# Optimization experiments

Hardware: AMD Instinct MI355X
Metric: run time of the kernel (lower is better)

The kernel has to match this reference:

```python
import jax, jax.numpy as jnp
import numpy as np

N_META, M_SUB = 64, 1024          # n meta-nodes, m nodes per sub-graph
D_IN, D_HID, D_OUT = 128, 128, 64
NUM_LAYERS_EXTRA, K = 2, 3        # total DSGraphGLayers = NUM_LAYERS_EXTRA + 1
N_EDGES = 1048576                 # ~avg degree 16 over 65536 nodes


def setup_inputs() -> dict:
    key = jax.random.key(0)
    ks = jax.random.split(key, 8)
    N = N_META * M_SUB
    x = jax.random.normal(ks[0], (N_META, M_SUB, D_IN), jnp.float32)
    sub_adj = jax.random.randint(ks[1], (2, N_EDGES), 0, N, dtype=jnp.int32)
    # dense binary meta-graph adjacency (n, n)
    adj = (jax.random.uniform(ks[2], (N_META, N_META)) < 0.1).astype(jnp.float32)
    L = NUM_LAYERS_EXTRA + 1
    scale = 1.0 / np.sqrt(D_HID).astype(np.float32)
    gcn_W = jax.random.normal(ks[3], (L, K + 1, D_HID, D_HID), jnp.float32) * scale
    gcn_b = jnp.zeros((L, K + 1, D_HID), jnp.float32)
    lin_W1 = jax.random.normal(ks[4], (D_HID, D_HID), jnp.float32) * scale
    lin_b1 = jnp.zeros((D_HID,), jnp.float32)
    lin_W2 = jax.random.normal(ks[5], (D_HID, D_OUT), jnp.float32) * scale
    lin_b2 = jnp.zeros((D_OUT,), jnp.float32)
    return dict(x=x, sub_adj=sub_adj, adj=adj, gcn_W=gcn_W, gcn_b=gcn_b,
                lin_W1=lin_W1, lin_b1=lin_b1, lin_W2=lin_W2, lin_b2=lin_b2)


def _gcn_conv(x, src, dst, dinv, W, b, N):
    norm = dinv[src] * dinv[dst]                      # [E+N]
    msg = (x @ W)[src] * norm[:, None]                # [E+N, d_out]
    return jax.ops.segment_sum(msg, dst, num_segments=N) + b


def reference(x, sub_adj, adj, gcn_W, gcn_b, lin_W1, lin_b1, lin_W2, lin_b2):
    n, m, d = x.shape
    N = n * m
    loops = jnp.arange(N, dtype=sub_adj.dtype)
    src = jnp.concatenate([sub_adj[0], loops])
    dst = jnp.concatenate([sub_adj[1], loops])
    deg = jax.ops.segment_sum(jnp.ones(src.shape, x.dtype), dst, num_segments=N)
    dinv = jnp.where(deg > 0, jax.lax.rsqrt(deg), jnp.zeros_like(deg))
    # precompute_adj: cached_adj = [adj, adj^2, ..., adj^K]; powers >= 2 detached in source
    cached = [adj]
    A = adj
    for _ in range(K - 1):
        A = jax.lax.stop_gradient(A @ adj)
        cached.append(A)
    for li in range(gcn_W.shape[0]):
        xf = x.reshape(N, -1)
        out = _gcn_conv(xf, src, dst, dinv, gcn_W[li, 0], gcn_b[li, 0], N)
        for i, Ai in enumerate(cached):
            # meta-graph mixing: x_i[n,m,d] = sum_j A_i[n,j] * x[j,m,d]
            xi = jnp.einsum('nj,jmd->nmd', Ai, x).reshape(N, -1)
            out = out + _gcn_conv(xi, src, dst, dinv, gcn_W[li, i + 1], gcn_b[li, i + 1], N)
        x = jax.nn.relu(out.reshape(n, m, -1))
    h = x.reshape(N, -1)
    h = jax.nn.relu(h @ lin_W1 + lin_b1)
    h = h @ lin_W2 + lin_b2
    return h.reshape(n, m, -1)
```

## Files before the change

kernel.cpp:

```cpp
#include <hip/hip_runtime.h>

#define NMETA 64
#define MSUB 1024
#define NNODES 65536
#define D 128
#define DOUT 64
#define NEDGES 1048576
#define COLS 131072
#define BCAP 5120

typedef __attribute__((ext_vector_type(8))) short bf8_t;
typedef __attribute__((ext_vector_type(4))) float f4_t;
typedef __attribute__((ext_vector_type(2))) float f2_t;

__device__ inline unsigned short bfr(float x) {
    unsigned u = __builtin_bit_cast(unsigned, x);
    u += 0x7fffu + ((u >> 16) & 1u);
    return (unsigned short)(u >> 16);
}
__device__ inline float b2f(unsigned short h) {
    return __builtin_bit_cast(float, (unsigned)h << 16);
}
__device__ inline f2_t up2(unsigned u) {
    f2_t r;
    r[0] = __builtin_bit_cast(float, u << 16);
    r[1] = __builtin_bit_cast(float, u & 0xffff0000u);
    return r;
}

__global__ __launch_bounds__(256) void k_bhist(const int* __restrict__ dst,
                                               int* __restrict__ whist) {
    __shared__ int c[256];
    int t = threadIdx.x, w = blockIdx.x;
    c[t] = 0;
    __syncthreads();
    const int* dp = dst + w * 4096;
    for (int k = 0; k < 16; ++k) atomicAdd(&c[dp[k * 256 + t] >> 8], 1);
    __syncthreads();
    whist[t * 256 + w] = c[t];
}

__global__ __launch_bounds__(256) void k_bscan(int* __restrict__ whist,
                                               int* __restrict__ bbase) {
    __shared__ int sh[256];
    int t = threadIdx.x;
    int run = 0;
    for (int w = 0; w < 256; ++w) {
        int v = whist[t * 256 + w];
        whist[t * 256 + w] = run;
        run += v;
    }
    sh[t] = run;
    __syncthreads();
    for (int d = 1; d < 256; d <<= 1) {
        int x = (t >= d) ? sh[t - d] : 0;
        __syncthreads();
        sh[t] += x;
        __syncthreads();
    }
    bbase[t] = sh[t] - run;
    if (t == 255) bbase[256] = NEDGES;
}

__global__ __launch_bounds__(256) void k_bscatter(const int* __restrict__ src,
                                                  const int* __restrict__ dst,
                                                  const int* __restrict__ bbase,
                                                  const int* __restrict__ whist,
                                                  unsigned* __restrict__ tmp) {
    __shared__ int cur[256];
    __shared__ int base[256];
    int t = threadIdx.x, w = blockIdx.x;
    cur[t] = 0;
    base[t] = bbase[t] + whist[t * 256 + w];
    __syncthreads();
    const int* dp = dst + w * 4096;
    const int* sp = src + w * 4096;
    for (int k = 0; k < 16; ++k) {
        int d = dp[k * 256 + t], s = sp[k * 256 + t];
        int b = d >> 8;
        int lr = atomicAdd(&cur[b], 1);
        tmp[base[b] + lr] = ((unsigned)(d & 255) << 16) | (unsigned)s;
    }
}

__global__ __launch_bounds__(256) void k_bcsr(const unsigned* __restrict__ tmp,
                                              const int* __restrict__ bbase,
                                              int* __restrict__ offs,
                                              float* __restrict__ dinv,
                                              unsigned short* __restrict__ csr16) {
    __shared__ unsigned pairs[BCAP];
    __shared__ unsigned short image[BCAP];
    __shared__ int cnt[256], cur[256], sh[256];
    int t = threadIdx.x, b = blockIdx.x;
    int base = bbase[b], n = bbase[b + 1] - base;
    for (int i = t; i < n; i += 256) pairs[i] = tmp[base + i];
    cnt[t] = 0;
    __syncthreads();
    for (int i = t; i < n; i += 256) atomicAdd(&cnt[pairs[i] >> 16], 1);
    __syncthreads();
    int c = cnt[t];
    sh[t] = c;
    __syncthreads();
    for (int d = 1; d < 256; d <<= 1) {
        int x = (t >= d) ? sh[t - d] : 0;
        __syncthreads();
        sh[t] += x;
        __syncthreads();
    }
    int excl = sh[t] - c;
    cur[t] = excl;
    offs[b * 256 + t] = base + excl;
    dinv[b * 256 + t] = rsqrtf((float)(c + 1));
    if (b == 255 && t == 255) offs[65536] = NEDGES;
    __syncthreads();
    for (int i = t; i < n; i += 256) {
        unsigned p = pairs[i];
        int pos = atomicAdd(&cur[p >> 16], 1);
        image[pos] = (unsigned short)(p & 0xffffu);
    }
    __syncthreads();
    for (int i = t; i < n; i += 256) csr16[base + i] = image[i];
}

__global__ __launch_bounds__(256) void k_setup(const float* __restrict__ A,
                                               unsigned short* __restrict__ Ab,
                                               const float4* __restrict__ x,
                                               ushort4* __restrict__ xo,
                                               const float* __restrict__ gcnW,
                                               const float* __restrict__ W1,
                                               const float* __restrict__ W2,
                                               unsigned short* __restrict__ Wt) {
    int blk = blockIdx.x, t = threadIdx.x;
    if (blk == 0) {
        __shared__ float As[4096];
        __shared__ float Bs[4096];
        for (int q = 0; q < 16; ++q) As[t + 256 * q] = A[t + 256 * q];
        __syncthreads();
        for (int q = 0; q < 16; ++q) {
            int idx = t + 256 * q;
            int n = idx >> 6, j = idx & 63;
            Ab[idx] = bfr(As[idx]);
            float acc = 0.f;
            for (int k = 0; k < 64; ++k) acc += As[n * 64 + k] * As[k * 64 + j];
            Bs[idx] = acc;
            Ab[4096 + idx] = bfr(acc);
        }
        __syncthreads();
        for (int q = 0; q < 16; ++q) {
            int idx = t + 256 * q;
            int n = idx >> 6, j = idx & 63;
            float acc = 0.f;
            for (int k = 0; k < 64; ++k) acc += Bs[n * 64 + k] * As[k * 64 + j];
            Ab[8192 + idx] = bfr(acc);
        }
    } else if (blk <= 8192) {
        int i = (blk - 1) * 256 + t;
        float4 v = x[i];
        ushort4 u;
        u.x = bfr(v.x); u.y = bfr(v.y); u.z = bfr(v.z); u.w = bfr(v.w);
        xo[i] = u;
    } else {
        int b2 = blk - 8193;
        int m = b2 >> 6;
        int idx = (b2 & 63) * 256 + t;
        const float* src;
        int N = 128;
        if (m < 12)       src = gcnW + m * 16384;
        else if (m == 12) src = W1;
        else { src = W2; N = 64; if (idx >= 8192) return; }
        int n = idx >> 7, k = idx & 127;
        Wt[m * 16384 + idx] = bfr(src[k * N + n]);
    }
}

#define TS 130
__global__ __launch_bounds__(256) void k_layer(const unsigned short* __restrict__ X,
                                               const unsigned short* __restrict__ Ab,
                                               const unsigned short* __restrict__ Wt4,
                                               unsigned short* __restrict__ Y) {
    __shared__ unsigned short LB[3 * 64 * TS];
    int t = threadIdx.x;
    int m = blockIdx.x;
    int wave = t >> 6, lane = t & 63;
    int l16 = lane & 15, kg = lane >> 4;
    int c0 = wave * 32;

#pragma unroll
    for (int it = 0; it < 4; ++it) {
        int slot = it * 256 + t;
        int row = slot >> 4, ch = slot & 15;
        *(uint4*)&LB[row * 128 + ch * 8] =
            *(const uint4*)(X + ((long)row * MSUB + m) * D + ch * 8);
    }
    __syncthreads();

    bf8_t xa[4][4];
#pragma unroll
    for (int mt = 0; mt < 4; ++mt)
#pragma unroll
        for (int kb = 0; kb < 4; ++kb)
            xa[mt][kb] = *(const bf8_t*)&LB[(mt * 16 + l16) * 128 + kb * 32 + kg * 8];
    __syncthreads();

    f4_t zero4 = {0.f, 0.f, 0.f, 0.f};

    f4_t accT0[4][2];
#pragma unroll
    for (int mt = 0; mt < 4; ++mt)
#pragma unroll
        for (int nt = 0; nt < 2; ++nt) accT0[mt][nt] = zero4;
#pragma unroll
    for (int kb = 0; kb < 4; ++kb)
#pragma unroll
        for (int nt = 0; nt < 2; ++nt) {
            bf8_t b = *(const bf8_t*)(Wt4 + (long)(c0 + nt * 16 + l16) * 128 +
                                      kb * 32 + kg * 8);
#pragma unroll
            for (int mt = 0; mt < 4; ++mt)
                accT0[mt][nt] = __builtin_amdgcn_mfma_f32_16x16x32_bf16(
                    xa[mt][kb], b, accT0[mt][nt], 0, 0, 0);
        }

#pragma unroll
    for (int z = 1; z < 4; ++z) {
        f4_t acc[4][2];
#pragma unroll
        for (int mt = 0; mt < 4; ++mt)
#pragma unroll
            for (int nt = 0; nt < 2; ++nt) acc[mt][nt] = zero4;
        const unsigned short* wp = Wt4 + z * 16384;
#pragma unroll
        for (int kb = 0; kb < 4; ++kb)
#pragma unroll
            for (int nt = 0; nt < 2; ++nt) {
                bf8_t b = *(const bf8_t*)(wp + (long)(c0 + nt * 16 + l16) * 128 +
                                          kb * 32 + kg * 8);
#pragma unroll
                for (int mt = 0; mt < 4; ++mt)
                    acc[mt][nt] = __builtin_amdgcn_mfma_f32_16x16x32_bf16(
                        xa[mt][kb], b, acc[mt][nt], 0, 0, 0);
            }
#pragma unroll
        for (int mt = 0; mt < 4; ++mt)
#pragma unroll
            for (int nt = 0; nt < 2; ++nt)
#pragma unroll
                for (int r = 0; r < 4; ++r)
                    LB[((z - 1) * 64 + mt * 16 + kg * 4 + r) * TS +
                       c0 + nt * 16 + l16] = bfr(acc[mt][nt][r]);
    }

    f4_t acc2[4][2];
#pragma unroll
    for (int mt = 0; mt < 4; ++mt)
#pragma unroll
        for (int nt = 0; nt < 2; ++nt) acc2[mt][nt] = zero4;
#pragma unroll
    for (int i = 0; i < 3; ++i)
#pragma unroll
        for (int kb = 0; kb < 2; ++kb) {
            bf8_t af[4];
#pragma unroll
            for (int mt = 0; mt < 4; ++mt)
                af[mt] = *(const bf8_t*)(Ab + i * 4096 + (mt * 16 + l16) * 64 +
                                         kb * 32 + kg * 8);
#pragma unroll
            for (int nt = 0; nt < 2; ++nt) {
                bf8_t b;
#pragma unroll
                for (int jj = 0; jj < 8; ++jj)
                    b[jj] = (short)LB[(i * 64 + kb * 32 + kg * 8 + jj) * TS +
                                      c0 + nt * 16 + l16];
#pragma unroll
                for (int mt = 0; mt < 4; ++mt)
                    acc2[mt][nt] = __builtin_amdgcn_mfma_f32_16x16x32_bf16(
                        af[mt], b, acc2[mt][nt], 0, 0, 0);
            }
        }

#pragma unroll
    for (int mt = 0; mt < 4; ++mt)
#pragma unroll
        for (int nt = 0; nt < 2; ++nt)
#pragma unroll
            for (int r = 0; r < 4; ++r) {
                int row = mt * 16 + kg * 4 + r;
                int col = c0 + nt * 16 + l16;
                float v = acc2[mt][nt][r] + accT0[mt][nt][r];
                Y[((long)row * MSUB + m) * D + col] = bfr(v);
            }
}

template <int NT, bool RELU, bool OUT_BF16>
__global__ __launch_bounds__(256) void k_mfma(const unsigned short* __restrict__ X,
                                              const unsigned short* __restrict__ Wt,
                                              const float* __restrict__ bias,
                                              void* __restrict__ Cout) {
    int wave = threadIdx.x >> 6, lane = threadIdx.x & 63;
    int l16 = lane & 15, kg = lane >> 4;
    long row0 = (long)blockIdx.x * 128 + wave * 32;
    const int NCOL = NT * 16;

    bf8_t a[2][4];
    const unsigned short* xp = X + row0 * 128 + kg * 8;
#pragma unroll
    for (int kb = 0; kb < 4; ++kb) {
        a[0][kb] = *(const bf8_t*)(xp + (long)l16 * 128 + kb * 32);
        a[1][kb] = *(const bf8_t*)(xp + (long)(l16 + 16) * 128 + kb * 32);
    }
    f4_t acc[2][NT];
    f4_t zero4 = {0.f, 0.f, 0.f, 0.f};
#pragma unroll
    for (int mt = 0; mt < 2; ++mt)
#pragma unroll
        for (int nt = 0; nt < NT; ++nt) acc[mt][nt] = zero4;

    const unsigned short* wp = Wt + (long)l16 * 128 + kg * 8;
#pragma unroll
    for (int kb = 0; kb < 4; ++kb)
#pragma unroll
        for (int nt = 0; nt < NT; ++nt) {
            bf8_t b = *(const bf8_t*)(wp + nt * 16 * 128 + kb * 32);
            acc[0][nt] = __builtin_amdgcn_mfma_f32_16x16x32_bf16(a[0][kb], b, acc[0][nt], 0, 0, 0);
            acc[1][nt] = __builtin_amdgcn_mfma_f32_16x16x32_bf16(a[1][kb], b, acc[1][nt], 0, 0, 0);
        }
#pragma unroll
    for (int mt = 0; mt < 2; ++mt)
#pragma unroll
        for (int nt = 0; nt < NT; ++nt)
#pragma unroll
            for (int r = 0; r < 4; ++r) {
                long row = row0 + mt * 16 + kg * 4 + r;
                int col = nt * 16 + l16;
                float v = acc[mt][nt][r] + bias[col];
                if (RELU) v = fmaxf(v, 0.f);
                long o = row * NCOL + col;
                if (OUT_BF16) ((unsigned short*)Cout)[o] = bfr(v);
                else          ((float*)Cout)[o] = v;
            }
}

__global__ __launch_bounds__(256) void k_prop(const unsigned short* __restrict__ Y,
                                              const int* __restrict__ offs,
                                              const unsigned short* __restrict__ csr,
                                              const float* __restrict__ dinv,
                                              const float* __restrict__ bias4,
                                              unsigned short* __restrict__ Xout) {
    int wid = threadIdx.x >> 6;
    int lane = threadIdx.x & 63;
    int q = lane >> 4;
    int l = lane & 15;
    int v = blockIdx.x * 4 + wid;
    const uint4* Y4 = (const uint4*)Y;
    int e0 = offs[v], e1 = offs[v + 1];
    f2_t acc2[4];
#pragma unroll
    for (int k = 0; k < 4; ++k) acc2[k] = (f2_t){0.f, 0.f};

    int e = e0 + q;
    for (; e + 4 < e1; e += 8) {
        int u0 = csr[e], u1 = csr[e + 4];
        float d0 = dinv[u0], d1 = dinv[u1];
        uint4 y0 = Y4[(long)u0 * 16 + l];
        uint4 y1 = Y4[(long)u1 * 16 + l];
        f2_t dd0 = {d0, d0}, dd1 = {d1, d1};
        acc2[0] += dd0 * up2(y0.x) + dd1 * up2(y1.x);
        acc2[1] += dd0 * up2(y0.y) + dd1 * up2(y1.y);
        acc2[2] += dd0 * up2(y0.z) + dd1 * up2(y1.z);
        acc2[3] += dd0 * up2(y0.w) + dd1 * up2(y1.w);
    }
    if (e < e1) {
        int u = csr[e];
        float du = dinv[u];
        uint4 y = Y4[(long)u * 16 + l];
        f2_t dd = {du, du};
        acc2[0] += dd * up2(y.x);
        acc2[1] += dd * up2(y.y);
        acc2[2] += dd * up2(y.z);
        acc2[3] += dd * up2(y.w);
    }
    float acc[8];
#pragma unroll
    for (int k = 0; k < 4; ++k) { acc[2 * k] = acc2[k][0]; acc[2 * k + 1] = acc2[k][1]; }
#pragma unroll
    for (int k = 0; k < 8; ++k) {
        acc[k] += __shfl_xor(acc[k], 32, 64);
        acc[k] += __shfl_xor(acc[k], 16, 64);
    }
    if (q == 0) {
        float dv = dinv[v];
        float dvv = dv * dv;
        uint4 s = Y4[(long)v * 16 + l];
        f2_t s2[4] = {up2(s.x), up2(s.y), up2(s.z), up2(s.w)};
        float bs[8];
#pragma unroll
        for (int k = 0; k < 8; ++k) bs[k] = 0.f;
#pragma unroll
        for (int p = 0; p < 4; ++p) {
            float4 blo = *(const float4*)(bias4 + p * 128 + l * 8);
            float4 bhi = *(const float4*)(bias4 + p * 128 + l * 8 + 4);
            bs[0] += blo.x; bs[1] += blo.y; bs[2] += blo.z; bs[3] += blo.w;
            bs[4] += bhi.x; bs[5] += bhi.y; bs[6] += bhi.z; bs[7] += bhi.w;
        }
        unsigned r[8];
#pragma unroll
        for (int k = 0; k < 8; ++k) {
            float sf = s2[k / 2][k % 2];
            r[k] = bfr(fmaxf(dv * acc[k] + dvv * sf + bs[k], 0.f));
        }
        uint4 pk;
        pk.x = (r[1] << 16) | r[0];
        pk.y = (r[3] << 16) | r[2];
        pk.z = (r[5] << 16) | r[4];
        pk.w = (r[7] << 16) | r[6];
        ((uint4*)Xout)[(long)v * 16 + l] = pk;
    }
}

extern "C" void kernel_launch(void* const* d_in, const int* in_sizes, int n_in,
                              void* d_out, int out_size, void* d_ws, size_t ws_size,
                              hipStream_t stream) {
    const float* x      = (const float*)d_in[0];
    const int*   subadj = (const int*)d_in[1];
    const float* adj    = (const float*)d_in[2];
    const float* gcn_W  = (const float*)d_in[3];
    const float* gcn_b  = (const float*)d_in[4];
    const float* lin_W1 = (const float*)d_in[5];
    const float* lin_b1 = (const float*)d_in[6];
    const float* lin_W2 = (const float*)d_in[7];
    const float* lin_b2 = (const float*)d_in[8];
    float* out = (float*)d_out;

    const int* e_src = subadj;
    const int* e_dst = subadj + NEDGES;

    char* w = (char*)d_ws;
    int*      whist = (int*)w;      w += (size_t)65536 * 4;
    int*      bbase = (int*)w;      w += (size_t)260 * 4;
    int*      offs  = (int*)w;      w += (size_t)65540 * 4;
    float*    dinv  = (float*)w;    w += (size_t)65536 * 4;
    unsigned* tmp   = (unsigned*)w; w += (size_t)NEDGES * 4;
    unsigned short* csr16 = (unsigned short*)w; w += (size_t)NEDGES * 2;
    unsigned short* Ab  = (unsigned short*)w; w += (size_t)3 * 4096 * 2;
    unsigned short* Xbf = (unsigned short*)w; w += (size_t)NNODES * D * 2;
    unsigned short* Ybf = (unsigned short*)w; w += (size_t)NNODES * D * 2;
    unsigned short* Wt  = (unsigned short*)w; w += (size_t)14 * 16384 * 2;
    unsigned short* Hbf = (unsigned short*)w; w += (size_t)NNODES * D * 2;

    k_bhist<<<256, 256, 0, stream>>>(e_dst, whist);
    k_bscan<<<1, 256, 0, stream>>>(whist, bbase);
    k_bscatter<<<256, 256, 0, stream>>>(e_src, e_dst, bbase, whist, tmp);
    k_bcsr<<<256, 256, 0, stream>>>(tmp, bbase, offs, dinv, csr16);
    k_setup<<<9089, 256, 0, stream>>>(adj, Ab, (const float4*)x, (ushort4*)Xbf,
                                      gcn_W, lin_W1, lin_W2, Wt);

    for (int li = 0; li < 3; ++li) {
        k_layer<<<MSUB, 256, 0, stream>>>(Xbf, Ab, Wt + (size_t)li * 4 * 16384, Ybf);
        k_prop<<<NNODES / 4, 256, 0, stream>>>(Ybf, offs, csr16, dinv,
                                               gcn_b + (size_t)li * 512, Xbf);
    }
    k_mfma<8, true, true><<<NNODES / 128, 256, 0, stream>>>(
        Xbf, Wt + (size_t)12 * 16384, lin_b1, Hbf);
    k_mfma<4, false, false><<<NNODES / 128, 256, 0, stream>>>(
        Hbf, Wt + (size_t)13 * 16384, lin_b2, out);
}
```

Measured before the change: 457.8 us.

## Fuse fp32-to-bf16 input conversion, prescale by dinv, and fuse MLP layers

Three changes. The fp32-to-bf16 conversion of x moves out of the setup kernel into the first layer's load. The source-side D^-1/2 normalization moves into the layer kernel's epilogue, so the edge-gather loop no longer loads dinv per neighbor, and that loop is unrolled to four neighbors. The two MLP GEMMs are fused into one kernel that keeps the hidden activations in shared memory. This removes a separate conversion pass, a random-access dinv load per edge, and a global round trip for H. The cost is an extra rounding of the prescaled Y to bf16 and more registers in the prop loop.

New measurement: 454.8 us. About the same (-0.7%).

```diff
diff --git a/kernel.cpp b/kernel.cpp
--- a/kernel.cpp
+++ b/kernel.cpp
@@ -124,8 +124,6 @@
 
 __global__ __launch_bounds__(256) void k_setup(const float* __restrict__ A,
                                                unsigned short* __restrict__ Ab,
-                                               const float4* __restrict__ x,
-                                               ushort4* __restrict__ xo,
                                                const float* __restrict__ gcnW,
                                                const float* __restrict__ W1,
                                                const float* __restrict__ W2,
@@ -153,14 +151,8 @@
             for (int k = 0; k < 64; ++k) acc += Bs[n * 64 + k] * As[k * 64 + j];
             Ab[8192 + idx] = bfr(acc);
         }
-    } else if (blk <= 8192) {
-        int i = (blk - 1) * 256 + t;
-        float4 v = x[i];
-        ushort4 u;
-        u.x = bfr(v.x); u.y = bfr(v.y); u.z = bfr(v.z); u.w = bfr(v.w);
-        xo[i] = u;
     } else {
-        int b2 = blk - 8193;
+        int b2 = blk - 1;
         int m = b2 >> 6;
         int idx = (b2 & 63) * 256 + t;
         const float* src;
@@ -174,23 +166,41 @@
 }
 
 #define TS 130
+template <bool INF32>
 __global__ __launch_bounds__(256) void k_layer(const unsigned short* __restrict__ X,
+                                               const float* __restrict__ Xf,
                                                const unsigned short* __restrict__ Ab,
                                                const unsigned short* __restrict__ Wt4,
+                                               const float* __restrict__ dinv,
                                                unsigned short* __restrict__ Y) {
     __shared__ unsigned short LB[3 * 64 * TS];
+    __shared__ float dsh[64];
     int t = threadIdx.x;
     int m = blockIdx.x;
     int wave = t >> 6, lane = t & 63;
     int l16 = lane & 15, kg = lane >> 4;
     int c0 = wave * 32;
 
+    if (t < 64) dsh[t] = dinv[(long)t * MSUB + m];
+
 #pragma unroll
     for (int it = 0; it < 4; ++it) {
         int slot = it * 256 + t;
         int row = slot >> 4, ch = slot & 15;
-        *(uint4*)&LB[row * 128 + ch * 8] =
-            *(const uint4*)(X + ((long)row * MSUB + m) * D + ch * 8);
+        if (INF32) {
+            const float* xp = Xf + ((long)row * MSUB + m) * D + ch * 8;
+            float4 va = *(const float4*)xp;
+            float4 vb = *(const float4*)(xp + 4);
+            uint4 pk;
+            pk.x = ((unsigned)bfr(va.y) << 16) | bfr(va.x);
+            pk.y = ((unsigned)bfr(va.w) << 16) | bfr(va.z);
+            pk.z = ((unsigned)bfr(vb.y) << 16) | bfr(vb.x);
+            pk.w = ((unsigned)bfr(vb.w) << 16) | bfr(vb.z);
+            *(uint4*)&LB[row * 128 + ch * 8] = pk;
+        } else {
+            *(uint4*)&LB[row * 128 + ch * 8] =
+                *(const uint4*)(X + ((long)row * MSUB + m) * D + ch * 8);
+        }
     }
     __syncthreads();
 
@@ -286,57 +296,8 @@
             for (int r = 0; r < 4; ++r) {
                 int row = mt * 16 + kg * 4 + r;
                 int col = c0 + nt * 16 + l16;
-                float v = acc2[mt][nt][r] + accT0[mt][nt][r];
+                float v = (acc2[mt][nt][r] + accT0[mt][nt][r]) * dsh[row];
                 Y[((long)row * MSUB + m) * D + col] = bfr(v);
-            }
-}
-
-template <int NT, bool RELU, bool OUT_BF16>
-__global__ __launch_bounds__(256) void k_mfma(const unsigned short* __restrict__ X,
-                                              const unsigned short* __restrict__ Wt,
-                                              const float* __restrict__ bias,
-                                              void* __restrict__ Cout) {
-    int wave = threadIdx.x >> 6, lane = threadIdx.x & 63;
-    int l16 = lane & 15, kg = lane >> 4;
-    long row0 = (long)blockIdx.x * 128 + wave * 32;
-    const int NCOL = NT * 16;
-
-    bf8_t a[2][4];
-    const unsigned short* xp = X + row0 * 128 + kg * 8;
-#pragma unroll
-    for (int kb = 0; kb < 4; ++kb) {
-        a[0][kb] = *(const bf8_t*)(xp + (long)l16 * 128 + kb * 32);
-        a[1][kb] = *(const bf8_t*)(xp + (long)(l16 + 16) * 128 + kb * 32);
-    }
-    f4_t acc[2][NT];
-    f4_t zero4 = {0.f, 0.f, 0.f, 0.f};
-#pragma unroll
-    for (int mt = 0; mt < 2; ++mt)
-#pragma unroll
-        for (int nt = 0; nt < NT; ++nt) acc[mt][nt] = zero4;
-
-    const unsigned short* wp = Wt + (long)l16 * 128 + kg * 8;
-#pragma unroll
-    for (int kb = 0; kb < 4; ++kb)
-#pragma unroll
-        for (int nt = 0; nt < NT; ++nt) {
-            bf8_t b = *(const bf8_t*)(wp + nt * 16 * 128 + kb * 32);
-            acc[0][nt] = __builtin_amdgcn_mfma_f32_16x16x32_bf16(a[0][kb], b, acc[0][nt], 0, 0, 0);
-            acc[1][nt] = __builtin_amdgcn_mfma_f32_16x16x32_bf16(a[1][kb], b, acc[1][nt], 0, 0, 0);
-        }
-#pragma unroll
-    for (int mt = 0; mt < 2; ++mt)
-#pragma unroll
-        for (int nt = 0; nt < NT; ++nt)
-#pragma unroll
-            for (int r = 0; r < 4; ++r) {
-                long row = row0 + mt * 16 + kg * 4 + r;
-                int col = nt * 16 + l16;
-                float v = acc[mt][nt][r] + bias[col];
-                if (RELU) v = fmaxf(v, 0.f);
-                long o = row * NCOL + col;
-                if (OUT_BF16) ((unsigned short*)Cout)[o] = bfr(v);
-                else          ((float*)Cout)[o] = v;
             }
 }
 
@@ -358,26 +319,34 @@
     for (int k = 0; k < 4; ++k) acc2[k] = (f2_t){0.f, 0.f};
 
     int e = e0 + q;
-    for (; e + 4 < e1; e += 8) {
-        int u0 = csr[e], u1 = csr[e + 4];
-        float d0 = dinv[u0], d1 = dinv[u1];
+    for (; e + 12 < e1; e += 16) {
+        int u0 = csr[e], u1 = csr[e + 4], u2 = csr[e + 8], u3 = csr[e + 12];
         uint4 y0 = Y4[(long)u0 * 16 + l];
         uint4 y1 = Y4[(long)u1 * 16 + l];
-        f2_t dd0 = {d0, d0}, dd1 = {d1, d1};
-        acc2[0] += dd0 * up2(y0.x) + dd1 * up2(y1.x);
-        acc2[1] += dd0 * up2(y0.y) + dd1 * up2(y1.y);
-        acc2[2] += dd0 * up2(y0.z) + dd1 * up2(y1.z);
-        acc2[3] += dd0 * up2(y0.w) + dd1 * up2(y1.w);
+        uint4 y2 = Y4[(long)u2 * 16 + l];
+        uint4 y3 = Y4[(long)u3 * 16 + l];
+        acc2[0] += (up2(y0.x) + up2(y1.x)) + (up2(y2.x) + up2(y3.x));
+        acc2[1] += (up2(y0.y) + up2(y1.y)) + (up2(y2.y) + up2(y3.y));
+        acc2[2] += (up2(y0.z) + up2(y1.z)) + (up2(y2.z) + up2(y3.z));
+        acc2[3] += (up2(y0.w) + up2(y1.w)) + (up2(y2.w) + up2(y3.w));
+    }
+    if (e + 4 < e1) {
+        int u0 = csr[e], u1 = csr[e + 4];
+        uint4 y0 = Y4[(long)u0 * 16 + l];
+        uint4 y1 = Y4[(long)u1 * 16 + l];
+        acc2[0] += up2(y0.x) + up2(y1.x);
+        acc2[1] += up2(y0.y) + up2(y1.y);
+        acc2[2] += up2(y0.z) + up2(y1.z);
+        acc2[3] += up2(y0.w) + up2(y1.w);
+        e += 8;
     }
     if (e < e1) {
         int u = csr[e];
-        float du = dinv[u];
         uint4 y = Y4[(long)u * 16 + l];
-        f2_t dd = {du, du};
-        acc2[0] += dd * up2(y.x);
-        acc2[1] += dd * up2(y.y);
-        acc2[2] += dd * up2(y.z);
-        acc2[3] += dd * up2(y.w);
+        acc2[0] += up2(y.x);
+        acc2[1] += up2(y.y);
+        acc2[2] += up2(y.z);
+        acc2[3] += up2(y.w);
     }
     float acc[8];
 #pragma unroll
@@ -389,7 +358,6 @@
     }
     if (q == 0) {
         float dv = dinv[v];
-        float dvv = dv * dv;
         uint4 s = Y4[(long)v * 16 + l];
         f2_t s2[4] = {up2(s.x), up2(s.y), up2(s.z), up2(s.w)};
         float bs[8];
@@ -406,7 +374,7 @@
 #pragma unroll
         for (int k = 0; k < 8; ++k) {
             float sf = s2[k / 2][k % 2];
-            r[k] = bfr(fmaxf(dv * acc[k] + dvv * sf + bs[k], 0.f));
+            r[k] = bfr(fmaxf(dv * (acc[k] + sf) + bs[k], 0.f));
         }
         uint4 pk;
         pk.x = (r[1] << 16) | r[0];
@@ -415,6 +383,86 @@
         pk.w = (r[7] << 16) | r[6];
         ((uint4*)Xout)[(long)v * 16 + l] = pk;
     }
+}
+
+#define HST 136
+__global__ __launch_bounds__(256) void k_mlp(const unsigned short* __restrict__ X,
+                                             const unsigned short* __restrict__ Wt,
+                                             const float* __restrict__ b1,
+                                             const float* __restrict__ b2,
+                                             float* __restrict__ out) {
+    __shared__ unsigned short H[128 * HST];
+    int wave = threadIdx.x >> 6, lane = threadIdx.x & 63;
+    int l16 = lane & 15, kg = lane >> 4;
+    long row0 = (long)blockIdx.x * 128 + wave * 32;
+    int hb = wave * 32 * HST;
+
+    bf8_t a[2][4];
+    const unsigned short* xp = X + row0 * 128 + kg * 8;
+#pragma unroll
+    for (int kb = 0; kb < 4; ++kb) {
+        a[0][kb] = *(const bf8_t*)(xp + (long)l16 * 128 + kb * 32);
+        a[1][kb] = *(const bf8_t*)(xp + (long)(l16 + 16) * 128 + kb * 32);
+    }
+    f4_t zero4 = {0.f, 0.f, 0.f, 0.f};
+    f4_t acc[2][8];
+#pragma unroll
+    for (int mt = 0; mt < 2; ++mt)
+#pragma unroll
+        for (int nt = 0; nt < 8; ++nt) acc[mt][nt] = zero4;
+
+    const unsigned short* wp = Wt + 12 * 16384 + (long)l16 * 128 + kg * 8;
+#pragma unroll
+    for (int kb = 0; kb < 4; ++kb)
+#pragma unroll
+        for (int nt = 0; nt < 8; ++nt) {
+            bf8_t b = *(const bf8_t*)(wp + nt * 16 * 128 + kb * 32);
+            acc[0][nt] = __builtin_amdgcn_mfma_f32_16x16x32_bf16(a[0][kb], b, acc[0][nt], 0, 0, 0);
+            acc[1][nt] = __builtin_amdgcn_mfma_f32_16x16x32_bf16(a[1][kb], b, acc[1][nt], 0, 0, 0);
+        }
+
+#pragma unroll
+    for (int nt = 0; nt < 8; ++nt) {
+        float bv = b1[nt * 16 + l16];
+#pragma unroll
+        for (int mt = 0; mt < 2; ++mt)
+#pragma unroll
+            for (int r = 0; r < 4; ++r) {
+                int row = mt * 16 + kg * 4 + r;
+                H[hb + row * HST + nt * 16 + l16] = bfr(fmaxf(acc[mt][nt][r] + bv, 0.f));
+            }
+    }
+
+    bf8_t h2[2][4];
+#pragma unroll
+    for (int kb = 0; kb < 4; ++kb) {
+        h2[0][kb] = *(const bf8_t*)&H[hb + l16 * HST + kb * 32 + kg * 8];
+        h2[1][kb] = *(const bf8_t*)&H[hb + (l16 + 16) * HST + kb * 32 + kg * 8];
+    }
+    f4_t acc2[2][4];
+#pragma unroll
+    for (int mt = 0; mt < 2; ++mt)
+#pragma unroll
+        for (int nt = 0; nt < 4; ++nt) acc2[mt][nt] = zero4;
+    const unsigned short* w2 = Wt + 13 * 16384 + (long)l16 * 128 + kg * 8;
+#pragma unroll
+    for (int kb = 0; kb < 4; ++kb)
+#pragma unroll
+        for (int nt = 0; nt < 4; ++nt) {
+            bf8_t b = *(const bf8_t*)(w2 + nt * 16 * 128 + kb * 32);
+            acc2[0][nt] = __builtin_amdgcn_mfma_f32_16x16x32_bf16(h2[0][kb], b, acc2[0][nt], 0, 0, 0);
+            acc2[1][nt] = __builtin_amdgcn_mfma_f32_16x16x32_bf16(h2[1][kb], b, acc2[1][nt], 0, 0, 0);
+        }
+#pragma unroll
+    for (int mt = 0; mt < 2; ++mt)
+#pragma unroll
+        for (int nt = 0; nt < 4; ++nt)
+#pragma unroll
+            for (int r = 0; r < 4; ++r) {
+                long row = row0 + mt * 16 + kg * 4 + r;
+                int col = nt * 16 + l16;
+                out[row * DOUT + col] = acc2[mt][nt][r] + b2[col];
+            }
 }
 
 extern "C" void kernel_launch(void* const* d_in, const int* in_sizes, int n_in,
@@ -445,22 +493,21 @@
     unsigned short* Xbf = (unsigned short*)w; w += (size_t)NNODES * D * 2;
     unsigned short* Ybf = (unsigned short*)w; w += (size_t)NNODES * D * 2;
     unsigned short* Wt  = (unsigned short*)w; w += (size_t)14 * 16384 * 2;
-    unsigned short* Hbf = (unsigned short*)w; w += (size_t)NNODES * D * 2;
 
     k_bhist<<<256, 256, 0, stream>>>(e_dst, whist);
     k_bscan<<<1, 256, 0, stream>>>(whist, bbase);
     k_bscatter<<<256, 256, 0, stream>>>(e_src, e_dst, bbase, whist, tmp);
     k_bcsr<<<256, 256, 0, stream>>>(tmp, bbase, offs, dinv, csr16);
-    k_setup<<<9089, 256, 0, stream>>>(adj, Ab, (const float4*)x, (ushort4*)Xbf,
-                                      gcn_W, lin_W1, lin_W2, Wt);
+    k_setup<<<897, 256, 0, stream>>>(adj, Ab, gcn_W, lin_W1, lin_W2, Wt);
 
     for (int li = 0; li < 3; ++li) {
-        k_layer<<<MSUB, 256, 0, stream>>>(Xbf, Ab, Wt + (size_t)li * 4 * 16384, Ybf);
+        if (li == 0)
+            k_layer<true><<<MSUB, 256, 0, stream>>>(nullptr, x, Ab, Wt, dinv, Ybf);
+        else
+            k_layer<false><<<MSUB, 256, 0, stream>>>(Xbf, nullptr, Ab,
+                                                     Wt + (size_t)li * 4 * 16384, dinv, Ybf);
         k_prop<<<NNODES / 4, 256, 0, stream>>>(Ybf, offs, csr16, dinv,
                                                gcn_b + (size_t)li * 512, Xbf);
     }
-    k_mfma<8, true, true><<<NNODES / 128, 256, 0, stream>>>(
-        Xbf, Wt + (size_t)12 * 16384, lin_b1, Hbf);
-    k_mfma<4, false, false><<<NNODES / 128, 256, 0, stream>>>(
-        Hbf, Wt + (size_t)13 * 16384, lin_b2, out);
-}
+    k_mlp<<<NNODES / 128, 256, 0, stream>>>(Xbf, Wt, lin_b1, lin_b2, out);
+}
```
